# Kernel optimization log

Measured on AMD Instinct MI355X. Metric: run time of the kernel, lower is better.

Reference implementation:

```python
import jax, jax.numpy as jnp
import numpy as np

E = 1024   # embed_dim
H = 16     # head_size
DH = E // H  # head_dim = 64
B, S = 2, 2048
SCALE = 1.0 / np.sqrt(E)  # original divides by sqrt(query.size(-1)) == sqrt(embed_dim)


def setup_inputs() -> dict:
    key = jax.random.key(0)
    ks = jax.random.split(key, 11)
    init = 0.02
    return {
        "query": jax.random.normal(ks[0], (B, S, E), dtype=jnp.float32),
        "key":   jax.random.normal(ks[1], (B, S, E), dtype=jnp.float32),
        "value": jax.random.normal(ks[2], (B, S, E), dtype=jnp.float32),
        # per-head projection weights, stacked over heads: [H, E, DH]
        "Wq": jax.random.normal(ks[3], (H, E, DH), dtype=jnp.float32) * init,
        "bq": jax.random.normal(ks[4], (H, DH), dtype=jnp.float32) * init,
        "Wk": jax.random.normal(ks[5], (H, E, DH), dtype=jnp.float32) * init,
        "bk": jax.random.normal(ks[6], (H, DH), dtype=jnp.float32) * init,
        "Wv": jax.random.normal(ks[7], (H, E, DH), dtype=jnp.float32) * init,
        "bv": jax.random.normal(ks[8], (H, DH), dtype=jnp.float32) * init,
        "Wo": jax.random.normal(ks[9], (E, E), dtype=jnp.float32) * init,
        "bo": jax.random.normal(ks[10], (E,), dtype=jnp.float32) * init,
    }


def reference(query, key, value, Wq, bq, Wk, bk, Wv, bv, Wo, bo):
    # per-head linear projections (vectorized over heads)
    q = jnp.einsum('bse,hed->bhsd', query, Wq) + bq[None, :, None, :]
    k = jnp.einsum('bse,hed->bhsd', key,   Wk) + bk[None, :, None, :]
    v = jnp.einsum('bse,hed->bhsd', value, Wv) + bv[None, :, None, :]
    # NOTE: original code scales by sqrt(embed_dim), not sqrt(head_dim)
    scores = jnp.einsum('bhqd,bhkd->bhqk', q, k) * SCALE
    weights = jax.nn.softmax(scores, axis=-1)
    out = jnp.einsum('bhqk,bhkd->bhqd', weights, v)  # [B,H,S,DH]
    # concat heads along last dim (head order == stacking order)
    out = out.transpose(0, 2, 1, 3).reshape(B, S, H * DH)
    return out @ Wo + bo
```

## Files before the change

### kernel.cpp

```cpp
#include <hip/hip_runtime.h>

typedef __bf16 bf16;
typedef __bf16 bf16x8 __attribute__((ext_vector_type(8)));
typedef __bf16 bf16x4 __attribute__((ext_vector_type(4)));
typedef float f32x4 __attribute__((ext_vector_type(4)));

#define MM 4096
#define NN 1024
#define KK 1024

__device__ __forceinline__ void gload_lds16(const void* g, void* l) {
  __builtin_amdgcn_global_load_lds(
      (const __attribute__((address_space(1))) void*)g,
      (__attribute__((address_space(3))) void*)l, 16, 0, 0);
}

__global__ __launch_bounds__(256) void cvt_x(const float* __restrict__ q,
                                             const float* __restrict__ k,
                                             const float* __restrict__ v,
                                             bf16* __restrict__ out)
{
  int p = blockIdx.y;
  const float* src = (p == 0) ? q : (p == 1 ? k : v);
  bf16* dst = out + (size_t)p * (MM * (size_t)KK);
  int i = (blockIdx.x * 256 + threadIdx.x) * 4;
  float4 val = *(const float4*)(src + i);
  bf16x4 o;
  o.x = (bf16)val.x; o.y = (bf16)val.y; o.z = (bf16)val.z; o.w = (bf16)val.w;
  *(bf16x4*)(dst + i) = o;
}

__global__ __launch_bounds__(256) void cvt_w(const float* __restrict__ Wq,
                                             const float* __restrict__ Wk,
                                             const float* __restrict__ Wv,
                                             const float* __restrict__ Wo,
                                             bf16* __restrict__ Wt,
                                             bf16* __restrict__ Wot)
{
  __shared__ bf16 Sl[64 * 72];
  const int t = threadIdx.x;
  const int bid = blockIdx.x;
  const int p = bid >> 8, t8 = bid & 255;
  const int ti = t >> 4, c4 = (t & 15) * 4;

  if (p < 3) {
    const float* W = (p == 0) ? Wq : (p == 1 ? Wk : Wv);
    const int h = t8 >> 4, e0 = (t8 & 15) << 6;
#pragma unroll
    for (int r = 0; r < 4; ++r) {
      int e_l = r * 16 + ti;
      float4 val = *(const float4*)(W + (h << 16) + (e0 + e_l) * 64 + c4);
      bf16x4 o; o.x = (bf16)val.x; o.y = (bf16)val.y; o.z = (bf16)val.z; o.w = (bf16)val.w;
      *(bf16x4*)(Sl + e_l * 72 + c4) = o;
    }
    __syncthreads();
#pragma unroll
    for (int r = 0; r < 4; ++r) {
      int d_l = r * 16 + ti;
      bf16x4 o;
      o.x = Sl[(c4 + 0) * 72 + d_l];
      o.y = Sl[(c4 + 1) * 72 + d_l];
      o.z = Sl[(c4 + 2) * 72 + d_l];
      o.w = Sl[(c4 + 3) * 72 + d_l];
      *(bf16x4*)(Wt + (size_t)p * 1048576 + (size_t)((h << 6) + d_l) * 1024 + e0 + c4) = o;
    }
  } else {
    const int n0 = (t8 >> 4) << 6, k0 = (t8 & 15) << 6;
#pragma unroll
    for (int r = 0; r < 4; ++r) {
      int k_l = r * 16 + ti;
      float4 val = *(const float4*)(Wo + (size_t)(k0 + k_l) * 1024 + n0 + c4);
      bf16x4 o; o.x = (bf16)val.x; o.y = (bf16)val.y; o.z = (bf16)val.z; o.w = (bf16)val.w;
      *(bf16x4*)(Sl + k_l * 72 + c4) = o;
    }
    __syncthreads();
#pragma unroll
    for (int r = 0; r < 4; ++r) {
      int n_l = r * 16 + ti;
      bf16x4 o;
      o.x = Sl[(c4 + 0) * 72 + n_l];
      o.y = Sl[(c4 + 1) * 72 + n_l];
      o.z = Sl[(c4 + 2) * 72 + n_l];
      o.w = Sl[(c4 + 3) * 72 + n_l];
      *(bf16x4*)(Wot + (size_t)(n0 + n_l) * 1024 + k0 + c4) = o;
    }
  }
}

__device__ __forceinline__ void gemm_body(const bf16* __restrict__ A,
                                          const bf16* __restrict__ Bt,
                                          bf16* As, bf16* Bs,
                                          int m0, int n0, f32x4 (&acc)[4][4])
{
  const int tid = threadIdx.x;
  const int w = tid >> 6, L = tid & 63;
  const int quad = L >> 4, l16 = L & 15;
  const int wm = (w & 1) << 6, wn = (w >> 1) << 6;

  const bf16* Ag = A + (size_t)(m0 + w * 32 + (L >> 2)) * KK + (L & 3) * 8;
  const bf16* Bg = Bt + (size_t)(n0 + w * 32 + (L >> 2)) * KK + (L & 3) * 8;
  bf16* Al = As + w * 1024;
  bf16* Bl = Bs + w * 1024;

  for (int kt = 0; kt < KK / 32; ++kt) {
    __syncthreads();
    const bf16* a0 = Ag + kt * 32;
    const bf16* b0 = Bg + kt * 32;
    gload_lds16(a0, Al);
    gload_lds16(a0 + 16 * KK, Al + 512);
    gload_lds16(b0, Bl);
    gload_lds16(b0 + 16 * KK, Bl + 512);
    __syncthreads();
    bf16x8 af[4], bfr[4];
#pragma unroll
    for (int mi = 0; mi < 4; ++mi)
      af[mi] = *(const bf16x8*)(As + (wm + mi * 16 + l16) * 32 + quad * 8);
#pragma unroll
    for (int ni = 0; ni < 4; ++ni)
      bfr[ni] = *(const bf16x8*)(Bs + (wn + ni * 16 + l16) * 32 + quad * 8);
#pragma unroll
    for (int mi = 0; mi < 4; ++mi)
#pragma unroll
      for (int ni = 0; ni < 4; ++ni)
        acc[mi][ni] = __builtin_amdgcn_mfma_f32_16x16x32_bf16(af[mi], bfr[ni],
                                                              acc[mi][ni], 0, 0, 0);
  }
}

__global__ __launch_bounds__(256) void gemm_proj(const bf16* __restrict__ X,
                                                 const bf16* __restrict__ Wt,
                                                 const float* __restrict__ b0,
                                                 const float* __restrict__ b1,
                                                 const float* __restrict__ b2,
                                                 bf16* __restrict__ Out)
{
  __shared__ bf16 As[4096], Bs[4096];
  int p = blockIdx.y;
  const bf16* A = X + (size_t)p * 4194304;
  const bf16* Bt = Wt + (size_t)p * 1048576;
  const float* bias = (p == 0) ? b0 : (p == 1 ? b1 : b2);
  bf16* C = Out + (size_t)p * 4194304;
  int bx = blockIdx.x;
  int m0 = (bx >> 3) << 7, n0 = (bx & 7) << 7;
  f32x4 acc[4][4] = {};
  gemm_body(A, Bt, As, Bs, m0, n0, acc);
  const int L = threadIdx.x & 63, w = threadIdx.x >> 6;
  const int quad = L >> 4, l16 = L & 15;
  const int wm = (w & 1) << 6, wn = (w >> 1) << 6;
#pragma unroll
  for (int ni = 0; ni < 4; ++ni) {
    int col = n0 + wn + ni * 16 + l16;
    float bv = bias[col];
#pragma unroll
    for (int mi = 0; mi < 4; ++mi)
#pragma unroll
      for (int r = 0; r < 4; ++r) {
        int row = m0 + wm + mi * 16 + quad * 4 + r;
        C[(size_t)row * NN + col] = (bf16)(acc[mi][ni][r] + bv);
      }
  }
}

__global__ __launch_bounds__(256) void gemm_outp(const bf16* __restrict__ A,
                                                 const bf16* __restrict__ Bt,
                                                 const float* __restrict__ bias,
                                                 float* __restrict__ C)
{
  __shared__ bf16 As[4096], Bs[4096];
  int bx = blockIdx.x;
  int m0 = (bx >> 3) << 7, n0 = (bx & 7) << 7;
  f32x4 acc[4][4] = {};
  gemm_body(A, Bt, As, Bs, m0, n0, acc);
  const int L = threadIdx.x & 63, w = threadIdx.x >> 6;
  const int quad = L >> 4, l16 = L & 15;
  const int wm = (w & 1) << 6, wn = (w >> 1) << 6;
#pragma unroll
  for (int ni = 0; ni < 4; ++ni) {
    int col = n0 + wn + ni * 16 + l16;
    float bv = bias[col];
#pragma unroll
    for (int mi = 0; mi < 4; ++mi)
#pragma unroll
      for (int r = 0; r < 4; ++r) {
        int row = m0 + wm + mi * 16 + quad * 4 + r;
        C[(size_t)row * NN + col] = acc[mi][ni][r] + bv;
      }
  }
}

__global__ __launch_bounds__(256) void flash_attn(const bf16* __restrict__ Qm,
                                                  const bf16* __restrict__ Km,
                                                  const bf16* __restrict__ Vm,
                                                  bf16* __restrict__ Om)
{
  __shared__ bf16 Kl[64 * 72];
  __shared__ bf16 Vt[64 * 72];
  __shared__ bf16 Pl[4][16 * 72];
  const int tid = threadIdx.x;
  const int w = tid >> 6, L = tid & 63;
  const int quad = L >> 4, l16 = L & 15;
  const int qb = blockIdx.x & 31;
  const int bh = blockIdx.x >> 5;
  const int b = bh >> 4, h = bh & 15;
  const int s0 = qb << 6;
  const size_t base = (size_t)b * 2048 * 1024 + h * 64;

  const bf16* qp = Qm + base + (size_t)(s0 + w * 16 + l16) * 1024 + quad * 8;
  bf16x8 qf0 = *(const bf16x8*)qp;
  bf16x8 qf1 = *(const bf16x8*)(qp + 32);
  const float SL = 0.03125f * 1.44269504088896f;
#pragma unroll
  for (int j = 0; j < 8; ++j) {
    qf0[j] = (bf16)((float)qf0[j] * SL);
    qf1[j] = (bf16)((float)qf1[j] * SL);
  }

  float l_i[4] = {0.f, 0.f, 0.f, 0.f};
  f32x4 oacc[4] = {};

  const int kcol = ((L & 15) << 2) | (L >> 4);
  const bf16* Kg = Km + base + (size_t)L * 1024 + w * 16;
  const bf16* Vg = Vm + base + (size_t)L * 1024 + w * 16;

  bf16x8 k0 = *(const bf16x8*)Kg;
  bf16x8 k1 = *(const bf16x8*)(Kg + 8);
  bf16x8 v0 = *(const bf16x8*)Vg;
  bf16x8 v1 = *(const bf16x8*)(Vg + 8);

  for (int kt = 0; kt < 32; ++kt) {
    __syncthreads();
    *(bf16x8*)(Kl + L * 72 + w * 16) = k0;
    *(bf16x8*)(Kl + L * 72 + w * 16 + 8) = k1;
#pragma unroll
    for (int j = 0; j < 8; ++j) {
      Vt[(w * 16 + j) * 72 + kcol] = v0[j];
      Vt[(w * 16 + 8 + j) * 72 + kcol] = v1[j];
    }
    if (kt + 1 < 32) {
      const bf16* kg = Kg + (size_t)(kt + 1) * 65536;
      const bf16* vg = Vg + (size_t)(kt + 1) * 65536;
      k0 = *(const bf16x8*)kg;
      k1 = *(const bf16x8*)(kg + 8);
      v0 = *(const bf16x8*)vg;
      v1 = *(const bf16x8*)(vg + 8);
    }
    __syncthreads();

    f32x4 sacc[4];
#pragma unroll
    for (int ns = 0; ns < 4; ++ns) {
      bf16x8 kf0 = *(const bf16x8*)(Kl + (ns * 16 + l16) * 72 + quad * 8);
      bf16x8 kf1 = *(const bf16x8*)(Kl + (ns * 16 + l16) * 72 + 32 + quad * 8);
      f32x4 s = {0.f, 0.f, 0.f, 0.f};
      s = __builtin_amdgcn_mfma_f32_16x16x32_bf16(qf0, kf0, s, 0, 0, 0);
      s = __builtin_amdgcn_mfma_f32_16x16x32_bf16(qf1, kf1, s, 0, 0, 0);
      sacc[ns] = s;
    }

#pragma unroll
    for (int r = 0; r < 4; ++r) {
      float p0 = exp2f(sacc[0][r]);
      float p1 = exp2f(sacc[1][r]);
      float p2 = exp2f(sacc[2][r]);
      float p3 = exp2f(sacc[3][r]);
      l_i[r] += (p0 + p1) + (p2 + p3);
      bf16x4 pv;
      pv.x = (bf16)p0; pv.y = (bf16)p1; pv.z = (bf16)p2; pv.w = (bf16)p3;
      *(bf16x4*)(&Pl[w][(quad * 4 + r) * 72 + l16 * 4]) = pv;
    }
    asm volatile("s_waitcnt lgkmcnt(0)" ::: "memory");
    bf16x8 pf0 = *(const bf16x8*)(&Pl[w][l16 * 72 + quad * 8]);
    bf16x8 pf1 = *(const bf16x8*)(&Pl[w][l16 * 72 + 32 + quad * 8]);
#pragma unroll
    for (int ds = 0; ds < 4; ++ds) {
      bf16x8 vf0 = *(const bf16x8*)(Vt + (ds * 16 + l16) * 72 + quad * 8);
      bf16x8 vf1 = *(const bf16x8*)(Vt + (ds * 16 + l16) * 72 + 32 + quad * 8);
      oacc[ds] = __builtin_amdgcn_mfma_f32_16x16x32_bf16(pf0, vf0, oacc[ds], 0, 0, 0);
      oacc[ds] = __builtin_amdgcn_mfma_f32_16x16x32_bf16(pf1, vf1, oacc[ds], 0, 0, 0);
    }
  }

#pragma unroll
  for (int r = 0; r < 4; ++r) {
    float l = l_i[r];
    l += __shfl_xor(l, 1);
    l += __shfl_xor(l, 2);
    l += __shfl_xor(l, 4);
    l += __shfl_xor(l, 8);
    float inv = 1.f / l;
    bf16* op = Om + base + (size_t)(s0 + w * 16 + quad * 4 + r) * 1024;
#pragma unroll
    for (int ds = 0; ds < 4; ++ds)
      op[ds * 16 + l16] = (bf16)(oacc[ds][r] * inv);
  }
}

extern "C" void kernel_launch(void* const* d_in, const int* in_sizes, int n_in,
                              void* d_out, int out_size, void* d_ws, size_t ws_size,
                              hipStream_t stream)
{
  const float* q  = (const float*)d_in[0];
  const float* k  = (const float*)d_in[1];
  const float* v  = (const float*)d_in[2];
  const float* Wq = (const float*)d_in[3];
  const float* bq = (const float*)d_in[4];
  const float* Wk = (const float*)d_in[5];
  const float* bk = (const float*)d_in[6];
  const float* Wv = (const float*)d_in[7];
  const float* bv = (const float*)d_in[8];
  const float* Wo = (const float*)d_in[9];
  const float* bo = (const float*)d_in[10];

  char* ws = (char*)d_ws;
  bf16* Xb  = (bf16*)ws;
  bf16* Wt  = (bf16*)(ws + 25165824);
  bf16* Wot = (bf16*)(ws + 31457280);
  bf16* QKV = (bf16*)(ws + 33554432);
  bf16* O   = (bf16*)ws;

  cvt_x<<<dim3(4096, 3), 256, 0, stream>>>(q, k, v, Xb);
  cvt_w<<<dim3(1024), 256, 0, stream>>>(Wq, Wk, Wv, Wo, Wt, Wot);
  gemm_proj<<<dim3(256, 3), 256, 0, stream>>>(Xb, Wt, bq, bk, bv, QKV);
  flash_attn<<<dim3(1024), 256, 0, stream>>>(QKV, QKV + 4194304, QKV + 8388608, O);
  gemm_outp<<<dim3(256), 256, 0, stream>>>(O, Wot, bo, (float*)d_out);
}
```

Measured before the change: 259.8 us.

## Merge conversion kernels, halve output GEMM tile, pack V transpose stores, use fast exp2

Merges the input and weight conversion kernels into a single launch to remove one kernel boundary. The output-projection GEMM now uses 64x128 tiles with its own inline loop, doubling the grid to 512 blocks so more CUs are busy. The flash-attention V transpose now pairs two keys per thread so each LDS write stores a bf16x2 instead of a single element. exp2f is replaced with the hardware exp2 builtin. Smaller GEMM tiles lower data reuse per block, and the builtin exp2 may differ slightly in precision.

```diff
diff --git a/kernel.cpp b/kernel.cpp
--- a/kernel.cpp
+++ b/kernel.cpp
@@ -3,6 +3,7 @@
 typedef __bf16 bf16;
 typedef __bf16 bf16x8 __attribute__((ext_vector_type(8)));
 typedef __bf16 bf16x4 __attribute__((ext_vector_type(4)));
+typedef __bf16 bf16x2 __attribute__((ext_vector_type(2)));
 typedef float f32x4 __attribute__((ext_vector_type(4)));
 
 #define MM 4096
@@ -15,32 +16,35 @@
       (__attribute__((address_space(3))) void*)l, 16, 0, 0);
 }
 
-__global__ __launch_bounds__(256) void cvt_x(const float* __restrict__ q,
-                                             const float* __restrict__ k,
-                                             const float* __restrict__ v,
-                                             bf16* __restrict__ out)
-{
-  int p = blockIdx.y;
-  const float* src = (p == 0) ? q : (p == 1 ? k : v);
-  bf16* dst = out + (size_t)p * (MM * (size_t)KK);
-  int i = (blockIdx.x * 256 + threadIdx.x) * 4;
-  float4 val = *(const float4*)(src + i);
-  bf16x4 o;
-  o.x = (bf16)val.x; o.y = (bf16)val.y; o.z = (bf16)val.z; o.w = (bf16)val.w;
-  *(bf16x4*)(dst + i) = o;
-}
-
-__global__ __launch_bounds__(256) void cvt_w(const float* __restrict__ Wq,
-                                             const float* __restrict__ Wk,
-                                             const float* __restrict__ Wv,
-                                             const float* __restrict__ Wo,
-                                             bf16* __restrict__ Wt,
-                                             bf16* __restrict__ Wot)
+__global__ __launch_bounds__(256) void cvt_all(const float* __restrict__ q,
+                                               const float* __restrict__ k,
+                                               const float* __restrict__ v,
+                                               const float* __restrict__ Wq,
+                                               const float* __restrict__ Wk,
+                                               const float* __restrict__ Wv,
+                                               const float* __restrict__ Wo,
+                                               bf16* __restrict__ Xb,
+                                               bf16* __restrict__ Wt,
+                                               bf16* __restrict__ Wot)
 {
   __shared__ bf16 Sl[64 * 72];
+  const int bid = blockIdx.x;
   const int t = threadIdx.x;
-  const int bid = blockIdx.x;
-  const int p = bid >> 8, t8 = bid & 255;
+
+  if (bid < 12288) {
+    int p = bid >> 12, bx = bid & 4095;
+    const float* src = (p == 0) ? q : (p == 1 ? k : v);
+    bf16* dst = Xb + (size_t)p * (MM * (size_t)KK);
+    int i = (bx * 256 + t) * 4;
+    float4 val = *(const float4*)(src + i);
+    bf16x4 o;
+    o.x = (bf16)val.x; o.y = (bf16)val.y; o.z = (bf16)val.z; o.w = (bf16)val.w;
+    *(bf16x4*)(dst + i) = o;
+    return;
+  }
+
+  const int wb = bid - 12288;
+  const int p = wb >> 8, t8 = wb & 255;
   const int ti = t >> 4, c4 = (t & 15) * 4;
 
   if (p < 3) {
@@ -166,20 +170,49 @@
                                                  const float* __restrict__ bias,
                                                  float* __restrict__ C)
 {
-  __shared__ bf16 As[4096], Bs[4096];
-  int bx = blockIdx.x;
-  int m0 = (bx >> 3) << 7, n0 = (bx & 7) << 7;
-  f32x4 acc[4][4] = {};
-  gemm_body(A, Bt, As, Bs, m0, n0, acc);
-  const int L = threadIdx.x & 63, w = threadIdx.x >> 6;
+  __shared__ bf16 As[2048], Bs[4096];
+  const int bx = blockIdx.x;
+  const int m0 = (bx >> 3) << 6, n0 = (bx & 7) << 7;
+  const int tid = threadIdx.x;
+  const int w = tid >> 6, L = tid & 63;
   const int quad = L >> 4, l16 = L & 15;
-  const int wm = (w & 1) << 6, wn = (w >> 1) << 6;
+  const int wm = (w & 1) << 5, wn = (w >> 1) << 6;
+
+  const bf16* Ag = A + (size_t)(m0 + w * 16 + (L >> 2)) * KK + (L & 3) * 8;
+  const bf16* Bg = Bt + (size_t)(n0 + w * 32 + (L >> 2)) * KK + (L & 3) * 8;
+  bf16* Al = As + w * 512;
+  bf16* Bl = Bs + w * 1024;
+
+  f32x4 acc[2][4] = {};
+  for (int kt = 0; kt < KK / 32; ++kt) {
+    __syncthreads();
+    const bf16* a0 = Ag + kt * 32;
+    const bf16* b0 = Bg + kt * 32;
+    gload_lds16(a0, Al);
+    gload_lds16(b0, Bl);
+    gload_lds16(b0 + 16 * KK, Bl + 512);
+    __syncthreads();
+    bf16x8 af[2], bfr[4];
+#pragma unroll
+    for (int mi = 0; mi < 2; ++mi)
+      af[mi] = *(const bf16x8*)(As + (wm + mi * 16 + l16) * 32 + quad * 8);
+#pragma unroll
+    for (int ni = 0; ni < 4; ++ni)
+      bfr[ni] = *(const bf16x8*)(Bs + (wn + ni * 16 + l16) * 32 + quad * 8);
+#pragma unroll
+    for (int mi = 0; mi < 2; ++mi)
+#pragma unroll
+      for (int ni = 0; ni < 4; ++ni)
+        acc[mi][ni] = __builtin_amdgcn_mfma_f32_16x16x32_bf16(af[mi], bfr[ni],
+                                                              acc[mi][ni], 0, 0, 0);
+  }
+
 #pragma unroll
   for (int ni = 0; ni < 4; ++ni) {
     int col = n0 + wn + ni * 16 + l16;
     float bv = bias[col];
 #pragma unroll
-    for (int mi = 0; mi < 4; ++mi)
+    for (int mi = 0; mi < 2; ++mi)
 #pragma unroll
       for (int r = 0; r < 4; ++r) {
         int row = m0 + wm + mi * 16 + quad * 4 + r;
@@ -218,14 +251,18 @@
   float l_i[4] = {0.f, 0.f, 0.f, 0.f};
   f32x4 oacc[4] = {};
 
-  const int kcol = ((L & 15) << 2) | (L >> 4);
   const bf16* Kg = Km + base + (size_t)L * 1024 + w * 16;
-  const bf16* Vg = Vm + base + (size_t)L * 1024 + w * 16;
+  const int p = L & 31;
+  const int kp = (p & 15) | ((p >> 4) << 5);
+  const int dh8 = w * 16 + ((L >> 5) << 3);
+  const int skp = ((kp & 15) << 2) | (kp >> 4);
+  const bf16* Vg0 = Vm + base + (size_t)kp * 1024 + dh8;
+  const bf16* Vg1 = Vg0 + 16 * 1024;
 
   bf16x8 k0 = *(const bf16x8*)Kg;
   bf16x8 k1 = *(const bf16x8*)(Kg + 8);
-  bf16x8 v0 = *(const bf16x8*)Vg;
-  bf16x8 v1 = *(const bf16x8*)(Vg + 8);
+  bf16x8 va = *(const bf16x8*)Vg0;
+  bf16x8 vb = *(const bf16x8*)Vg1;
 
   for (int kt = 0; kt < 32; ++kt) {
     __syncthreads();
@@ -233,16 +270,14 @@
     *(bf16x8*)(Kl + L * 72 + w * 16 + 8) = k1;
 #pragma unroll
     for (int j = 0; j < 8; ++j) {
-      Vt[(w * 16 + j) * 72 + kcol] = v0[j];
-      Vt[(w * 16 + 8 + j) * 72 + kcol] = v1[j];
+      bf16x2 pr; pr.x = va[j]; pr.y = vb[j];
+      *(bf16x2*)(Vt + (dh8 + j) * 72 + skp) = pr;
     }
     if (kt + 1 < 32) {
-      const bf16* kg = Kg + (size_t)(kt + 1) * 65536;
-      const bf16* vg = Vg + (size_t)(kt + 1) * 65536;
-      k0 = *(const bf16x8*)kg;
-      k1 = *(const bf16x8*)(kg + 8);
-      v0 = *(const bf16x8*)vg;
-      v1 = *(const bf16x8*)(vg + 8);
+      k0 = *(const bf16x8*)(Kg + (size_t)(kt + 1) * 65536);
+      k1 = *(const bf16x8*)(Kg + (size_t)(kt + 1) * 65536 + 8);
+      va = *(const bf16x8*)(Vg0 + (size_t)(kt + 1) * 65536);
+      vb = *(const bf16x8*)(Vg1 + (size_t)(kt + 1) * 65536);
     }
     __syncthreads();
 
@@ -259,10 +294,10 @@
 
 #pragma unroll
     for (int r = 0; r < 4; ++r) {
-      float p0 = exp2f(sacc[0][r]);
-      float p1 = exp2f(sacc[1][r]);
-      float p2 = exp2f(sacc[2][r]);
-      float p3 = exp2f(sacc[3][r]);
+      float p0 = __builtin_amdgcn_exp2f(sacc[0][r]);
+      float p1 = __builtin_amdgcn_exp2f(sacc[1][r]);
+      float p2 = __builtin_amdgcn_exp2f(sacc[2][r]);
+      float p3 = __builtin_amdgcn_exp2f(sacc[3][r]);
       l_i[r] += (p0 + p1) + (p2 + p3);
       bf16x4 pv;
       pv.x = (bf16)p0; pv.y = (bf16)p1; pv.z = (bf16)p2; pv.w = (bf16)p3;
@@ -318,9 +353,8 @@
   bf16* QKV = (bf16*)(ws + 33554432);
   bf16* O   = (bf16*)ws;
 
-  cvt_x<<<dim3(4096, 3), 256, 0, stream>>>(q, k, v, Xb);
-  cvt_w<<<dim3(1024), 256, 0, stream>>>(Wq, Wk, Wv, Wo, Wt, Wot);
+  cvt_all<<<dim3(13312), 256, 0, stream>>>(q, k, v, Wq, Wk, Wv, Wo, Xb, Wt, Wot);
   gemm_proj<<<dim3(256, 3), 256, 0, stream>>>(Xb, Wt, bq, bk, bv, QKV);
   flash_attn<<<dim3(1024), 256, 0, stream>>>(QKV, QKV + 4194304, QKV + 8388608, O);
-  gemm_outp<<<dim3(256), 256, 0, stream>>>(O, Wot, bo, (float*)d_out);
-}
+  gemm_outp<<<dim3(512), 256, 0, stream>>>(O, Wot, bo, (float*)d_out);
+}
```

Result: faster. 247.6 us (-4.7%).
